# Kernel tuning notes

Hardware: AMD Instinct MI355X
Metric: run time of the kernel (lower is better)

Reference implementation:

```python
import jax, jax.numpy as jnp
import numpy as np

VOCAB, EMB, HID = 32000, 512, 1024
BATCH, SEQ = 32, 512


def setup_inputs() -> dict:
    key = jax.random.key(0)
    ks = jax.random.split(key, 5)
    scale_e = 1.0 / np.sqrt(EMB)
    scale_h = 1.0 / np.sqrt(HID)
    return {
        "source": jax.random.randint(ks[0], (BATCH, SEQ), 0, VOCAB, dtype=jnp.int64),
        "embedding": jax.random.normal(ks[1], (VOCAB, EMB), dtype=jnp.float32),
        "W_ih": jax.random.normal(ks[2], (EMB, 4 * HID), dtype=jnp.float32) * scale_e,
        "W_hh": jax.random.normal(ks[3], (HID, 4 * HID), dtype=jnp.float32) * scale_h,
        "b_ih": jnp.zeros((4 * HID,), dtype=jnp.float32),
        "b_hh": jnp.zeros((4 * HID,), dtype=jnp.float32),
    }


def _lstm_forward(source, embedding, W_ih, W_hh, b_ih, b_hh):
    B, S = source.shape
    H = W_hh.shape[0]
    embedded = embedding[source]                      # [B, S, E]
    # Precompute input contributions for all timesteps in one big GEMM.
    x_gates = jnp.einsum("bse,eg->bsg", embedded, W_ih) + b_ih + b_hh  # [B, S, 4H]

    def step(carry, xg_t):
        h, c = carry
        gates = xg_t + h @ W_hh                       # [B, 4H]
        i, f, g, o = jnp.split(gates, 4, axis=-1)
        i = jax.nn.sigmoid(i)
        f = jax.nn.sigmoid(f)
        g = jnp.tanh(g)
        o = jax.nn.sigmoid(o)
        c_new = f * c + i * g
        h_new = o * jnp.tanh(c_new)
        return (h_new, c_new), h_new

    h0 = jnp.zeros((B, H), dtype=embedded.dtype)
    c0 = jnp.zeros((B, H), dtype=embedded.dtype)
    # scan over time: [S, B, 4H]
    _, hiddens = jax.lax.scan(step, (h0, c0), jnp.swapaxes(x_gates, 0, 1))
    return jnp.swapaxes(hiddens, 0, 1)                # [B, S, H]


def reference(source, embedding, W_ih, W_hh, b_ih, b_hh):
    return _lstm_forward(source, embedding, W_ih, W_hh, b_ih, b_hh)
```

## Files before the change

### kernel.cpp

```cpp
#include <hip/hip_runtime.h>
#include <math.h>


#define B_ 32
#define S_ 512
#define E_ 512
#define H_ 1024
#define G_ 4096
#define NWG 256
#define RTHR 512
#define BH_ (B_ * H_)
#define XGPAD 40

typedef _Float16 f16x8 __attribute__((ext_vector_type(8)));
typedef _Float16 f16x4 __attribute__((ext_vector_type(4)));
typedef float f32x4 __attribute__((ext_vector_type(4)));

__device__ __forceinline__ float sigmoidf_(float x) {
  return 1.0f / (1.0f + __expf(-x));
}
__device__ __forceinline__ float tanhf_(float x) {
  return 1.0f - 2.0f / (__expf(2.0f * x) + 1.0f);
}

__global__ __launch_bounds__(256) void wt_kernel(
    const float* __restrict__ W, _Float16* __restrict__ Wt, int K)
{
  __shared__ float Lt[64][65];
  const int c0 = blockIdx.x * 64;
  const int k0 = blockIdx.y * 64;
  const int tid = threadIdx.x;
  const int colL = tid & 63;
  const int rq = tid >> 6;
#pragma unroll 4
  for (int p = 0; p < 16; ++p) {
    int r = p * 4 + rq;
    Lt[colL][r] = W[(size_t)(k0 + r) * G_ + c0 + colL];
  }
  __syncthreads();
  const int col = tid >> 2;
  const int kq = (tid & 3) * 16;
  _Float16 tmp[16];
#pragma unroll
  for (int i = 0; i < 16; ++i) tmp[i] = (_Float16)Lt[col][kq + i];
  *(f16x8*)(Wt + (size_t)(c0 + col) * K + k0 + kq)     = *(f16x8*)&tmp[0];
  *(f16x8*)(Wt + (size_t)(c0 + col) * K + k0 + kq + 8) = *(f16x8*)&tmp[8];
}

__global__ __launch_bounds__(128) void gather_a(
    const int* __restrict__ src, const float* __restrict__ emb,
    _Float16* __restrict__ A, int t0)
{
  const int r = blockIdx.x;
  const int t = t0 + (r >> 5), b = r & 31;
  const int vrow = src[b * S_ + t];
  const float4 v = *(const float4*)(emb + (size_t)vrow * E_ + threadIdx.x * 4);
  f16x4 o = { (_Float16)v.x, (_Float16)v.y, (_Float16)v.z, (_Float16)v.w };
  *(f16x4*)(A + (size_t)r * E_ + threadIdx.x * 4) = o;
}

__global__ __launch_bounds__(256) void xgates_mfma(
    const _Float16* __restrict__ A, const _Float16* __restrict__ Bw,
    const float* __restrict__ bih, const float* __restrict__ bhh,
    _Float16* __restrict__ xg)
{
  __shared__ _Float16 Al[128][XGPAD];
  __shared__ _Float16 Bl[128][XGPAD];
  const int tid = threadIdx.x;
  const int row0 = blockIdx.y * 128;
  const int col0 = blockIdx.x * 128;
  const int wave = tid >> 6, lane = tid & 63;
  const int wm = wave >> 1, wn = wave & 1;
  const int lrow = lane & 15, lhi = lane >> 4;

  float bias[4];
#pragma unroll
  for (int n = 0; n < 4; ++n) {
    int c = col0 + wn * 64 + n * 16 + lrow;
    bias[n] = bih[c] + bhh[c];
  }
  f32x4 acc[4][4];
#pragma unroll
  for (int m = 0; m < 4; ++m)
#pragma unroll
    for (int n = 0; n < 4; ++n)
      acc[m][n] = (f32x4){bias[n], bias[n], bias[n], bias[n]};

  for (int kt = 0; kt < E_ / 32; ++kt) {
#pragma unroll
    for (int p = 0; p < 2; ++p) {
      int cch = tid * 2 + p;
      int rr = cch >> 2, kc = cch & 3;
      *(f16x8*)&Al[rr][kc * 8] =
          *(const f16x8*)(A + (size_t)(row0 + rr) * E_ + kt * 32 + kc * 8);
      *(f16x8*)&Bl[rr][kc * 8] =
          *(const f16x8*)(Bw + (size_t)(col0 + rr) * E_ + kt * 32 + kc * 8);
    }
    __syncthreads();
    f16x8 af[4], bfr[4];
#pragma unroll
    for (int m = 0; m < 4; ++m)
      af[m] = *(const f16x8*)&Al[wm * 64 + m * 16 + lrow][lhi * 8];
#pragma unroll
    for (int n = 0; n < 4; ++n)
      bfr[n] = *(const f16x8*)&Bl[wn * 64 + n * 16 + lrow][lhi * 8];
#pragma unroll
    for (int m = 0; m < 4; ++m)
#pragma unroll
      for (int n = 0; n < 4; ++n)
        acc[m][n] = __builtin_amdgcn_mfma_f32_16x16x32_f16(af[m], bfr[n],
                                                           acc[m][n], 0, 0, 0);
    __syncthreads();
  }
#pragma unroll
  for (int m = 0; m < 4; ++m)
#pragma unroll
    for (int n = 0; n < 4; ++n) {
      const int ccol = col0 + wn * 64 + n * 16 + lrow;
#pragma unroll
      for (int r = 0; r < 4; ++r) {
        const int rrow = row0 + wm * 64 + m * 16 + lhi * 4 + r;
        xg[(size_t)rrow * G_ + ccol] = (_Float16)acc[m][n][r];
      }
    }
}

__global__ __launch_bounds__(RTHR) void lstm_mfma(
    const _Float16* __restrict__ Wt, const _Float16* __restrict__ xg,
    unsigned short* hring, float* cbuf, unsigned* flg,
    float* out, int t0, int nt)
{
  __shared__ float red[8 * 32 * 17];

  const int wg = blockIdx.x;
  const int tid = threadIdx.x;
  const int J0 = 4 * ((wg & 7) * 32 + (wg >> 3));

  const int wave = tid >> 6;
  const int lane = tid & 63;
  const int lrow = lane & 15;
  const int lhi  = lane >> 4;
  const int Kw   = wave * 128;
  const int gcol = (lrow >> 2) * H_ + J0 + (lrow & 3);

  f16x8 bf[4];
#pragma unroll
  for (int s = 0; s < 4; ++s)
    bf[s] = *(const f16x8*)(Wt + (size_t)gcol * H_ + Kw + s * 32 + lhi * 8);

  const int bq = tid >> 2, jq = tid & 3;
  float cstate = 0.f;
  if (tid < 128) cstate = cbuf[(size_t)bq * H_ + J0 + jq];

  float xv0 = 0.f, xv1 = 0.f, xv2 = 0.f, xv3 = 0.f;
  if (tid < 128) {
    const _Float16* xp = xg + (size_t)bq * G_ + J0 + jq;
    xv0 = (float)xp[0];      xv1 = (float)xp[H_];
    xv2 = (float)xp[2 * H_]; xv3 = (float)xp[3 * H_];
  }

  for (int t = t0; t < t0 + nt; ++t) {
    const int lt = t - t0;
    const _Float16* hrd = (const _Float16*)hring + (size_t)lt * BH_;
    unsigned short* hwr = hring + (size_t)((lt == nt - 1) ? 0 : lt + 1) * BH_;

    if (wave == 0) {
      const unsigned* fp = flg + (size_t)t * 256 + lane * 4;
      int guard = 0;
      for (;;) {
        unsigned a0 = __hip_atomic_load(fp + 0, __ATOMIC_RELAXED, __HIP_MEMORY_SCOPE_AGENT);
        unsigned a1 = __hip_atomic_load(fp + 1, __ATOMIC_RELAXED, __HIP_MEMORY_SCOPE_AGENT);
        unsigned a2 = __hip_atomic_load(fp + 2, __ATOMIC_RELAXED, __HIP_MEMORY_SCOPE_AGENT);
        unsigned a3 = __hip_atomic_load(fp + 3, __ATOMIC_RELAXED, __HIP_MEMORY_SCOPE_AGENT);
        if (__all((a0 & a1 & a2 & a3) != 0u)) break;
        __builtin_amdgcn_s_sleep(1);
        if (++guard > (1 << 22)) break;
      }
    }
    __syncthreads();

    f32x4 acc0 = {0.f, 0.f, 0.f, 0.f};
    f32x4 acc1 = {0.f, 0.f, 0.f, 0.f};
#pragma unroll
    for (int s = 0; s < 4; ++s) {
      f16x8 a0 = *(const f16x8*)(hrd + (size_t)lrow * H_ + Kw + s * 32 + lhi * 8);
      f16x8 a1 = *(const f16x8*)(hrd + (size_t)(16 + lrow) * H_ + Kw + s * 32 + lhi * 8);
      acc0 = __builtin_amdgcn_mfma_f32_16x16x32_f16(a0, bf[s], acc0, 0, 0, 0);
      acc1 = __builtin_amdgcn_mfma_f32_16x16x32_f16(a1, bf[s], acc1, 0, 0, 0);
    }

    float xn0 = 0.f, xn1 = 0.f, xn2 = 0.f, xn3 = 0.f;
    if (tid < 128) {
      const int nlt = (lt == nt - 1) ? lt : lt + 1;
      const _Float16* xp = xg + ((size_t)nlt * B_ + bq) * G_ + J0 + jq;
      xn0 = (float)xp[0];      xn1 = (float)xp[H_];
      xn2 = (float)xp[2 * H_]; xn3 = (float)xp[3 * H_];
    }

#pragma unroll
    for (int r = 0; r < 4; ++r) {
      red[(wave * 32 + lhi * 4 + r) * 17 + lrow]      = acc0[r];
      red[(wave * 32 + 16 + lhi * 4 + r) * 17 + lrow] = acc1[r];
    }
    __syncthreads();

    if (tid < 128) {
      float g0 = xv0, g1 = xv1, g2 = xv2, g3 = xv3;
#pragma unroll
      for (int w = 0; w < 8; ++w) {
        const float* rp = red + (w * 32 + bq) * 17;
        g0 += rp[jq];
        g1 += rp[4 + jq];
        g2 += rp[8 + jq];
        g3 += rp[12 + jq];
      }
      float ig = sigmoidf_(g0);
      float fg = sigmoidf_(g1);
      float gg = tanhf_(g2);
      float og = sigmoidf_(g3);
      cstate = fg * cstate + ig * gg;
      float hval = og * tanhf_(cstate);
      out[((size_t)bq * S_ + t) * H_ + J0 + jq] = hval;
      _Float16 hf = (_Float16)hval;
      unsigned short hb;
      __builtin_memcpy(&hb, &hf, 2);
      __hip_atomic_store(hwr + (size_t)bq * H_ + J0 + jq, hb,
                         __ATOMIC_RELAXED, __HIP_MEMORY_SCOPE_AGENT);
    }
    __syncthreads();

    if (tid == 0)
      __hip_atomic_store(flg + (size_t)(t + 1) * 256 + wg, 1u,
                         __ATOMIC_RELAXED, __HIP_MEMORY_SCOPE_AGENT);

    xv0 = xn0; xv1 = xn1; xv2 = xn2; xv3 = xn3;
  }

  if (tid < 128) cbuf[(size_t)bq * H_ + J0 + jq] = cstate;
}

extern "C" void kernel_launch(void* const* d_in, const int* in_sizes, int n_in,
                              void* d_out, int out_size, void* d_ws, size_t ws_size,
                              hipStream_t stream) {
  const int*   src = (const int*)d_in[0];
  const float* emb = (const float*)d_in[1];
  const float* Wih = (const float*)d_in[2];
  const float* Whh = (const float*)d_in[3];
  const float* bih = (const float*)d_in[4];
  const float* bhh = (const float*)d_in[5];
  float* out = (float*)d_out;

  char* ws = (char*)d_ws;
  float*    cbuf = (float*)ws;
  unsigned* flg  = (unsigned*)(ws + 131072);
  const size_t stateBytes = 131072 + 525312;
  _Float16* Wt  = (_Float16*)(ws + stateBytes);
  _Float16* Wt2 = (_Float16*)(ws + stateBytes + 8388608);
  const size_t fixedBytes = stateBytes + 8388608 + 4194304;

  int chunk = 0;
  const int cand[4] = {512, 256, 128, 64};
  for (int ci = 0; ci < 4; ++ci) {
    size_t need = fixedBytes + (size_t)(cand[ci] + 1) * (BH_ * 2)
                  + (size_t)cand[ci] * B_ * E_ * 2
                  + (size_t)cand[ci] * B_ * G_ * 2;
    if (need <= ws_size) { chunk = cand[ci]; break; }
  }
  if (chunk == 0) return;

  unsigned short* hring = (unsigned short*)(ws + fixedBytes);
  _Float16* Af16 = (_Float16*)(ws + fixedBytes + (size_t)(chunk + 1) * (BH_ * 2));
  _Float16* xg   = (_Float16*)(ws + fixedBytes + (size_t)(chunk + 1) * (BH_ * 2)
                               + (size_t)chunk * B_ * E_ * 2);

  (void)hipMemsetAsync(ws, 0, stateBytes, stream);
  (void)hipMemsetAsync(flg, 1, 1024, stream);
  (void)hipMemsetAsync(hring, 0, BH_ * 2, stream);

  int K1 = H_, K2 = E_;
  wt_kernel<<<dim3(64, 16), 256, 0, stream>>>(Whh, Wt, K1);
  wt_kernel<<<dim3(64, 8), 256, 0, stream>>>(Wih, Wt2, K2);

  for (int t0 = 0; t0 < S_; t0 += chunk) {
    gather_a<<<dim3(chunk * B_), 128, 0, stream>>>(src, emb, Af16, t0);
    xgates_mfma<<<dim3(G_ / 128, chunk * B_ / 128), 256, 0, stream>>>(
        Af16, Wt2, bih, bhh, xg);

    int nt = chunk;
    void* args[] = {(void*)&Wt, (void*)&xg, (void*)&hring, (void*)&cbuf,
                    (void*)&flg, (void*)&out, (void*)&t0, (void*)&nt};
    (void)hipLaunchCooperativeKernel((void*)lstm_mfma, dim3(NWG), dim3(RTHR),
                                     args, 0u, stream);
  }
}
```

Measured before the change: 2.642 ms.

## Replace per-step workgroup barriers with LDS relay flag and per-wave arrival flags

The recurrent LSTM kernel drops two of its three __syncthreads per timestep. Wave 0 polls the global flags and signals the other waves through an LDS relay variable, and the reduction buffer is double-buffered to avoid write-after-read hazards. Each of the two writer waves now publishes its own arrival flag right after its h stores drain, so the flag array doubles and is polled as 64-bit words. The output store and next-step x-gate loads move after the flag publish, keeping them off the critical path. The trade is more spinning waves and subtle memory-ordering assumptions that rely on relaxed atomics and manual waitcnt.

```diff
diff --git a/kernel.cpp b/kernel.cpp
--- a/kernel.cpp
+++ b/kernel.cpp
@@ -15,6 +15,7 @@
 typedef _Float16 f16x8 __attribute__((ext_vector_type(8)));
 typedef _Float16 f16x4 __attribute__((ext_vector_type(4)));
 typedef float f32x4 __attribute__((ext_vector_type(4)));
+typedef unsigned long long u64;
 
 __device__ __forceinline__ float sigmoidf_(float x) {
   return 1.0f / (1.0f + __expf(-x));
@@ -125,12 +126,13 @@
     }
 }
 
-__global__ __launch_bounds__(RTHR) void lstm_mfma(
+__global__ __launch_bounds__(RTHR) void lstm_nb(
     const _Float16* __restrict__ Wt, const _Float16* __restrict__ xg,
     unsigned short* hring, float* cbuf, unsigned* flg,
     float* out, int t0, int nt)
 {
-  __shared__ float red[8 * 32 * 17];
+  __shared__ float red[2][8 * 32 * 17];
+  __shared__ int relay;
 
   const int wg = blockIdx.x;
   const int tid = threadIdx.x;
@@ -143,6 +145,9 @@
   const int Kw   = wave * 128;
   const int gcol = (lrow >> 2) * H_ + J0 + (lrow & 3);
 
+  if (tid == 0) relay = t0 - 1;
+  __syncthreads();
+
   f16x8 bf[4];
 #pragma unroll
   for (int s = 0; s < 4; ++s)
@@ -161,23 +166,37 @@
 
   for (int t = t0; t < t0 + nt; ++t) {
     const int lt = t - t0;
+    const int slot = t & 1;
     const _Float16* hrd = (const _Float16*)hring + (size_t)lt * BH_;
     unsigned short* hwr = hring + (size_t)((lt == nt - 1) ? 0 : lt + 1) * BH_;
 
     if (wave == 0) {
-      const unsigned* fp = flg + (size_t)t * 256 + lane * 4;
+      const u64* fq = (const u64*)flg + (size_t)t * 256;
       int guard = 0;
       for (;;) {
-        unsigned a0 = __hip_atomic_load(fp + 0, __ATOMIC_RELAXED, __HIP_MEMORY_SCOPE_AGENT);
-        unsigned a1 = __hip_atomic_load(fp + 1, __ATOMIC_RELAXED, __HIP_MEMORY_SCOPE_AGENT);
-        unsigned a2 = __hip_atomic_load(fp + 2, __ATOMIC_RELAXED, __HIP_MEMORY_SCOPE_AGENT);
-        unsigned a3 = __hip_atomic_load(fp + 3, __ATOMIC_RELAXED, __HIP_MEMORY_SCOPE_AGENT);
-        if (__all((a0 & a1 & a2 & a3) != 0u)) break;
+        u64 a0 = __hip_atomic_load(fq + lane,       __ATOMIC_RELAXED, __HIP_MEMORY_SCOPE_AGENT);
+        u64 a1 = __hip_atomic_load(fq + lane + 64,  __ATOMIC_RELAXED, __HIP_MEMORY_SCOPE_AGENT);
+        u64 a2 = __hip_atomic_load(fq + lane + 128, __ATOMIC_RELAXED, __HIP_MEMORY_SCOPE_AGENT);
+        u64 a3 = __hip_atomic_load(fq + lane + 192, __ATOMIC_RELAXED, __HIP_MEMORY_SCOPE_AGENT);
+        unsigned m = (unsigned)a0 & (unsigned)(a0 >> 32)
+                   & (unsigned)a1 & (unsigned)(a1 >> 32)
+                   & (unsigned)a2 & (unsigned)(a2 >> 32)
+                   & (unsigned)a3 & (unsigned)(a3 >> 32);
+        if (__all(m != 0u)) break;
         __builtin_amdgcn_s_sleep(1);
         if (++guard > (1 << 22)) break;
       }
-    }
-    __syncthreads();
+      if (lane == 0)
+        __hip_atomic_store(&relay, t, __ATOMIC_RELAXED, __HIP_MEMORY_SCOPE_WORKGROUP);
+    } else {
+      int guard = 0;
+      while (__hip_atomic_load(&relay, __ATOMIC_RELAXED,
+                               __HIP_MEMORY_SCOPE_WORKGROUP) < t) {
+        __builtin_amdgcn_s_sleep(1);
+        if (++guard > (1 << 22)) break;
+      }
+    }
+    asm volatile("" ::: "memory");
 
     f32x4 acc0 = {0.f, 0.f, 0.f, 0.f};
     f32x4 acc1 = {0.f, 0.f, 0.f, 0.f};
@@ -189,18 +208,10 @@
       acc1 = __builtin_amdgcn_mfma_f32_16x16x32_f16(a1, bf[s], acc1, 0, 0, 0);
     }
 
-    float xn0 = 0.f, xn1 = 0.f, xn2 = 0.f, xn3 = 0.f;
-    if (tid < 128) {
-      const int nlt = (lt == nt - 1) ? lt : lt + 1;
-      const _Float16* xp = xg + ((size_t)nlt * B_ + bq) * G_ + J0 + jq;
-      xn0 = (float)xp[0];      xn1 = (float)xp[H_];
-      xn2 = (float)xp[2 * H_]; xn3 = (float)xp[3 * H_];
-    }
-
 #pragma unroll
     for (int r = 0; r < 4; ++r) {
-      red[(wave * 32 + lhi * 4 + r) * 17 + lrow]      = acc0[r];
-      red[(wave * 32 + 16 + lhi * 4 + r) * 17 + lrow] = acc1[r];
+      red[slot][(wave * 32 + lhi * 4 + r) * 17 + lrow]      = acc0[r];
+      red[slot][(wave * 32 + 16 + lhi * 4 + r) * 17 + lrow] = acc1[r];
     }
     __syncthreads();
 
@@ -208,32 +219,35 @@
       float g0 = xv0, g1 = xv1, g2 = xv2, g3 = xv3;
 #pragma unroll
       for (int w = 0; w < 8; ++w) {
-        const float* rp = red + (w * 32 + bq) * 17;
+        const float* rp = &red[slot][(w * 32 + bq) * 17];
         g0 += rp[jq];
         g1 += rp[4 + jq];
         g2 += rp[8 + jq];
         g3 += rp[12 + jq];
       }
-      float ig = sigmoidf_(g0);
-      float fg = sigmoidf_(g1);
-      float gg = tanhf_(g2);
-      float og = sigmoidf_(g3);
+      const float ig = sigmoidf_(g0);
+      const float fg = sigmoidf_(g1);
+      const float gg = tanhf_(g2);
+      const float og = sigmoidf_(g3);
       cstate = fg * cstate + ig * gg;
-      float hval = og * tanhf_(cstate);
-      out[((size_t)bq * S_ + t) * H_ + J0 + jq] = hval;
-      _Float16 hf = (_Float16)hval;
+      const float hval = og * tanhf_(cstate);
+
+      const _Float16 hf = (_Float16)hval;
       unsigned short hb;
       __builtin_memcpy(&hb, &hf, 2);
       __hip_atomic_store(hwr + (size_t)bq * H_ + J0 + jq, hb,
                          __ATOMIC_RELAXED, __HIP_MEMORY_SCOPE_AGENT);
-    }
-    __syncthreads();
-
-    if (tid == 0)
-      __hip_atomic_store(flg + (size_t)(t + 1) * 256 + wg, 1u,
-                         __ATOMIC_RELAXED, __HIP_MEMORY_SCOPE_AGENT);
-
-    xv0 = xn0; xv1 = xn1; xv2 = xn2; xv3 = xn3;
+      asm volatile("s_waitcnt vmcnt(0)" ::: "memory");
+      if (lane == 0)
+        __hip_atomic_store(flg + (size_t)(t + 1) * 512 + wg * 2 + wave, 1u,
+                           __ATOMIC_RELAXED, __HIP_MEMORY_SCOPE_AGENT);
+
+      out[((size_t)bq * S_ + t) * H_ + J0 + jq] = hval;
+      const int nlt = (lt == nt - 1) ? lt : lt + 1;
+      const _Float16* xp = xg + ((size_t)nlt * B_ + bq) * G_ + J0 + jq;
+      xv0 = (float)xp[0];      xv1 = (float)xp[H_];
+      xv2 = (float)xp[2 * H_]; xv3 = (float)xp[3 * H_];
+    }
   }
 
   if (tid < 128) cbuf[(size_t)bq * H_ + J0 + jq] = cstate;
@@ -253,7 +267,7 @@
   char* ws = (char*)d_ws;
   float*    cbuf = (float*)ws;
   unsigned* flg  = (unsigned*)(ws + 131072);
-  const size_t stateBytes = 131072 + 525312;
+  const size_t stateBytes = 131072 + 1050624;
   _Float16* Wt  = (_Float16*)(ws + stateBytes);
   _Float16* Wt2 = (_Float16*)(ws + stateBytes + 8388608);
   const size_t fixedBytes = stateBytes + 8388608 + 4194304;
@@ -274,7 +288,7 @@
                                + (size_t)chunk * B_ * E_ * 2);
 
   (void)hipMemsetAsync(ws, 0, stateBytes, stream);
-  (void)hipMemsetAsync(flg, 1, 1024, stream);
+  (void)hipMemsetAsync(flg, 1, 2048, stream);
   (void)hipMemsetAsync(hring, 0, BH_ * 2, stream);
 
   int K1 = H_, K2 = E_;
@@ -289,7 +303,7 @@
     int nt = chunk;
     void* args[] = {(void*)&Wt, (void*)&xg, (void*)&hring, (void*)&cbuf,
                     (void*)&flg, (void*)&out, (void*)&t0, (void*)&nt};
-    (void)hipLaunchCooperativeKernel((void*)lstm_mfma, dim3(NWG), dim3(RTHR),
+    (void)hipLaunchCooperativeKernel((void*)lstm_nb, dim3(NWG), dim3(RTHR),
                                      args, 0u, stream);
   }
 }
```

New measurement: 2.831 ms. +7.2%, slower.
